# Performance work log

Hardware: AMD Instinct MI355X
Metric: run time of the kernel (lower is better)

The kernel has to match this reference:

```python
import jax, jax.numpy as jnp
import numpy as np

NE, NPROC, E, D = 50000, 25000, 200000, 128
L, T = 3, 4  # layers, edge types: 0:e->e, 1:e->p, 2:p->p, 3:p->e


def setup_inputs() -> dict:
    key = jax.random.key(0)
    ks = jax.random.split(key, 17)
    s = 1.0 / np.sqrt(D)
    return {
        'x_elem': jax.random.normal(ks[0], (NE, D), jnp.float32),
        'x_proc': jax.random.normal(ks[1], (NPROC, D), jnp.float32),
        'W_src': jax.random.normal(ks[2], (L, T, D, D), jnp.float32) * s,
        'W_dst': jax.random.normal(ks[3], (L, T, D, D), jnp.float32) * s,
        'att_src': jax.random.normal(ks[4], (L, T, D), jnp.float32) * s,
        'att_dst': jax.random.normal(ks[5], (L, T, D), jnp.float32) * s,
        'bias': jax.random.normal(ks[6], (L, T, D), jnp.float32) * 0.01,
        'lin_W': jax.random.normal(ks[7], (D, 2), jnp.float32) * s,
        'lin_b': jnp.zeros((2,), jnp.float32),
        'ee_src': jax.random.randint(ks[8], (E,), 0, NE),
        'ee_dst': jax.random.randint(ks[9], (E,), 0, NE),
        'ep_src': jax.random.randint(ks[10], (E,), 0, NE),
        'ep_dst': jax.random.randint(ks[11], (E,), 0, NPROC),
        'pp_src': jax.random.randint(ks[12], (E,), 0, NPROC),
        'pp_dst': jax.random.randint(ks[13], (E,), 0, NPROC),
        'pe_src': jax.random.randint(ks[14], (E,), 0, NPROC),
        'pe_dst': jax.random.randint(ks[15], (E,), 0, NE),
    }


def _gat(x_s, x_d, src, dst, n_dst, Ws, Wd, a_s, a_d, b):
    # one GATConv (heads=1, negative_slope=0 -> relu, no self loops)
    hs = x_s @ Ws                       # [Ns, D]
    hd = x_d @ Wd                       # [Nd, D]
    es = hs @ a_s                       # [Ns]
    ed = hd @ a_d                       # [Nd]
    logit = jax.nn.relu(es[src] + ed[dst])              # [E]
    m = jax.ops.segment_max(logit, dst, num_segments=n_dst)
    m = jnp.where(jnp.isfinite(m), m, 0.0)              # empty segments
    w = jnp.exp(logit - m[dst])
    denom = jax.ops.segment_sum(w, dst, num_segments=n_dst)
    alpha = w / jnp.maximum(denom[dst], 1e-16)          # edge softmax per dst
    out = jax.ops.segment_sum(alpha[:, None] * hs[src], dst, num_segments=n_dst)
    return out + b


def reference(x_elem, x_proc, W_src, W_dst, att_src, att_dst, bias, lin_W, lin_b,
              ee_src, ee_dst, ep_src, ep_dst, pp_src, pp_dst, pe_src, pe_dst):
    xe, xp = x_elem, x_proc
    for l in range(L):
        ee = _gat(xe, xe, ee_src, ee_dst, NE, W_src[l, 0], W_dst[l, 0], att_src[l, 0], att_dst[l, 0], bias[l, 0])
        ep = _gat(xe, xp, ep_src, ep_dst, NPROC, W_src[l, 1], W_dst[l, 1], att_src[l, 1], att_dst[l, 1], bias[l, 1])
        pp = _gat(xp, xp, pp_src, pp_dst, NPROC, W_src[l, 2], W_dst[l, 2], att_src[l, 2], att_dst[l, 2], bias[l, 2])
        pe = _gat(xp, xe, pe_src, pe_dst, NE, W_src[l, 3], W_dst[l, 3], att_src[l, 3], att_dst[l, 3], bias[l, 3])
        xe = ee + pe   # to_hetero aggr='sum' per destination node type
        xp = ep + pp
    x = jnp.concatenate([xe, xp], axis=0) @ lin_W + lin_b  # G_aggr
    return x.mean(axis=0)  # [2]
```

## Files before the change

### kernel.cpp

```cpp
#include <hip/hip_runtime.h>

#define NE_N 50000
#define NP_N 25000
#define E_N 200000
#define DIM 128
#define LOG2E 1.4426950408889634f
#define NREP 1024

#define NCHK 32
#define CHK_E (E_N / NCHK)
#define TBL 16384

typedef __attribute__((ext_vector_type(8))) short short8;
typedef __attribute__((ext_vector_type(4))) float f32x4;
typedef __attribute__((ext_vector_type(2))) float f32x2;

static __device__ __forceinline__ ushort f2bf(float f) {
  unsigned x = __float_as_uint(f);
  return (ushort)((x + 0x7fffu + ((x >> 16) & 1u)) >> 16);
}
static __device__ __forceinline__ float bf2f(ushort u) {
  return __uint_as_float(((unsigned)u) << 16);
}

#define HIST_BLKS (4 * NCHK)
#define HS_TOT (HIST_BLKS + 12 + 3)
__global__ __launch_bounds__(512) void hist_setup_k(
    const float* __restrict__ W_src, const float* __restrict__ W_dst,
    const float* __restrict__ att_dst, ushort* __restrict__ WbT,
    float* __restrict__ vec, const int* __restrict__ d0,
    const int* __restrict__ d1, const int* __restrict__ d2,
    const int* __restrict__ d3, unsigned char* __restrict__ h0,
    unsigned char* __restrict__ h1, unsigned char* __restrict__ h2,
    unsigned char* __restrict__ h3, ushort* __restrict__ rk0,
    ushort* __restrict__ rk1, ushort* __restrict__ rk2,
    ushort* __restrict__ rk3) {
  __shared__ int keys[TBL];
  __shared__ int cnts[TBL];
  const int blk = blockIdx.x;
  const int tid = threadIdx.x;
  if (blk < HIST_BLKS) {
    const int ty = blk >> 5, c = blk & (NCHK - 1);
    const int NN = (ty == 0 || ty == 3) ? NE_N : NP_N;
    const int* dst = ty == 0 ? d0 : ty == 1 ? d1 : ty == 2 ? d2 : d3;
    unsigned char* h = ty == 0 ? h0 : ty == 1 ? h1 : ty == 2 ? h2 : h3;
    ushort* rk = ty == 0 ? rk0 : ty == 1 ? rk1 : ty == 2 ? rk2 : rk3;
    for (int i = tid; i < TBL; i += 512) { keys[i] = -1; cnts[i] = 0; }
    __syncthreads();
    const int base = c * CHK_E;
    for (int i = tid; i < CHK_E; i += 512) {
      const int e = base + i;
      const int d = dst[e];
      unsigned hsh = ((unsigned)d * 2654435761u) >> 18;
      hsh &= (TBL - 1);
      int lr;
      while (true) {
        int prev = atomicCAS(&keys[hsh], -1, d);
        if (prev == -1 || prev == d) { lr = atomicAdd(&cnts[hsh], 1); break; }
        hsh = (hsh + 1) & (TBL - 1);
      }
      rk[e] = (ushort)lr;
    }
    __syncthreads();
    for (int i = tid; i < TBL; i += 512) {
      int k = keys[i];
      if (k >= 0) h[(size_t)c * NN + k] = (unsigned char)cnts[i];
    }
  } else if (blk < HIST_BLKS + 12) {
    const int w = blk - HIST_BLKS;
    const float* src = W_src + (size_t)w * DIM * DIM;
    ushort* dstw = WbT + (size_t)w * DIM * DIM;
    for (int i = tid; i < DIM * DIM; i += 512) {
      int k = i >> 7, n = i & 127;
      dstw[n * DIM + k] = f2bf(src[i]);
    }
  } else {
    const int b = blk - HIST_BLKS - 12;
    const int lt = b * 4 + (tid >> 7);
    const int i = tid & 127;
    const float* Wd = W_dst + (size_t)lt * DIM * DIM;
    const float* ad = att_dst + lt * DIM;
    float s = 0.f;
#pragma unroll 8
    for (int j = 0; j < DIM; j++) s += Wd[i * DIM + j] * ad[j];
    vec[lt * DIM + i] = s;
  }
}

__global__ __launch_bounds__(256) void scanA_k(
    unsigned char* __restrict__ h0, unsigned char* __restrict__ h1,
    unsigned char* __restrict__ h2, unsigned char* __restrict__ h3,
    int* __restrict__ c0, int* __restrict__ c1, int* __restrict__ c2,
    int* __restrict__ c3, int* __restrict__ part) {
  int ty = blockIdx.y;
  unsigned char* h = ty == 0 ? h0 : ty == 1 ? h1 : ty == 2 ? h2 : h3;
  int* cnt = ty == 0 ? c0 : ty == 1 ? c1 : ty == 2 ? c2 : c3;
  int n = (ty == 0 || ty == 3) ? NE_N : NP_N;
  int nblk = (n + 1023) >> 10;
  if ((int)blockIdx.x >= nblk) return;
  int base = blockIdx.x * 1024 + threadIdx.x * 4;
  int s = 0;
  if (base < n) {
    int run0 = 0, run1 = 0, run2 = 0, run3 = 0;
#pragma unroll
    for (int c = 0; c < NCHK; c++) {
      unsigned* hp = (unsigned*)(h + (size_t)c * n + base);
      unsigned v = *hp;
      *hp = (unsigned)(run0 & 255) | ((unsigned)(run1 & 255) << 8) |
            ((unsigned)(run2 & 255) << 16) | ((unsigned)(run3 & 255) << 24);
      run0 += (int)(v & 255u);
      run1 += (int)((v >> 8) & 255u);
      run2 += (int)((v >> 16) & 255u);
      run3 += (int)((v >> 24) & 255u);
    }
    cnt[base + 0] = run0; cnt[base + 1] = run1;
    cnt[base + 2] = run2; cnt[base + 3] = run3;
    s = run0 + run1 + run2 + run3;
  }
  int lane = threadIdx.x & 63, wid = threadIdx.x >> 6;
#pragma unroll
  for (int off = 32; off > 0; off >>= 1) s += __shfl_xor(s, off, 64);
  __shared__ int ws4[4];
  if (lane == 0) ws4[wid] = s;
  __syncthreads();
  if (threadIdx.x == 0)
    part[ty * 64 + blockIdx.x] = ws4[0] + ws4[1] + ws4[2] + ws4[3];
}

__global__ __launch_bounds__(256) void scanBC_k(
    const int* __restrict__ c0, const int* __restrict__ c1,
    const int* __restrict__ c2, const int* __restrict__ c3,
    int* __restrict__ r0, int* __restrict__ r1, int* __restrict__ r2,
    int* __restrict__ r3, const int* __restrict__ part) {
  int ty = blockIdx.y;
  int bx = blockIdx.x;
  const int* cnt = ty == 0 ? c0 : ty == 1 ? c1 : ty == 2 ? c2 : c3;
  int* rp = ty == 0 ? r0 : ty == 1 ? r1 : ty == 2 ? r2 : r3;
  int n = (ty == 0 || ty == 3) ? NE_N : NP_N;
  int nblk = (n + 1023) >> 10;
  if (bx >= nblk) return;

  __shared__ int s_excl;
  if (threadIdx.x < 64) {
    int pl = threadIdx.x;
    int v = (pl < nblk) ? part[ty * 64 + pl] : 0;
    int sc = v;
#pragma unroll
    for (int off = 1; off < 64; off <<= 1) {
      int t = __shfl_up(sc, off, 64);
      if (pl >= off) sc += t;
    }
    if (pl == bx) s_excl = sc - v;
  }
  if (bx == 0 && threadIdx.x == 0) rp[n] = E_N;
  __syncthreads();

  int base = bx * 1024 + threadIdx.x * 4;
  int v[4];
#pragma unroll
  for (int j = 0; j < 4; j++) v[j] = (base + j < n) ? cnt[base + j] : 0;
  int s = v[0] + v[1] + v[2] + v[3];
  int lane = threadIdx.x & 63, wid = threadIdx.x >> 6;
  int sc = s;
#pragma unroll
  for (int off = 1; off < 64; off <<= 1) {
    int t = __shfl_up(sc, off, 64);
    if (lane >= off) sc += t;
  }
  __shared__ int ws4[4];
  if (lane == 63) ws4[wid] = sc;
  __syncthreads();
  int wbase = 0;
  for (int w = 0; w < wid; w++) wbase += ws4[w];
  int p = s_excl + wbase + sc - s;
#pragma unroll
  for (int j = 0; j < 4; j++) {
    if (base + j < n) rp[base + j] = p;
    p += v[j];
  }
}

#define EBLK ((NE_N + 127) / 128)
#define PBLK ((NP_N + 127) / 128)
#define GEMM_BLK (EBLK + PBLK)
#define FILL_PER_CHK 13
#define FILL_BLKS (4 * NCHK * FILL_PER_CHK)
#define HG2_TOT (GEMM_BLK + FILL_BLKS)

template <bool FP32>
static __device__ __forceinline__ void gemm_body(
    int blk, const void* __restrict__ xev, const void* __restrict__ xpv,
    const ushort* __restrict__ WbT, const float* __restrict__ att,
    const float* __restrict__ vec, int l, unsigned char* __restrict__ hsE0,
    unsigned char* __restrict__ hsE1, unsigned char* __restrict__ hsP3,
    unsigned char* __restrict__ hsP2, float* __restrict__ esE0,
    float* __restrict__ esE1, float* __restrict__ esP3,
    float* __restrict__ esP2, float* __restrict__ edEA,
    float* __restrict__ edEB, float* __restrict__ edPA,
    float* __restrict__ edPB) {
  const void* xb;
  const ushort *W0T, *W1T;
  const float *a0, *a1, *dv0, *dv1;
  unsigned char *hs0, *hs1;
  float *es0, *es1, *edA, *edB;
  int N, rbase;
  if (blk < EBLK) {
    xb = xev; N = NE_N; rbase = blk * 128;
    W0T = WbT + (size_t)(l * 4 + 0) * DIM * DIM;
    W1T = WbT + (size_t)(l * 4 + 1) * DIM * DIM;
    a0 = att + (l * 4 + 0) * DIM; a1 = att + (l * 4 + 1) * DIM;
    dv0 = vec + (l * 4 + 0) * DIM; dv1 = vec + (l * 4 + 3) * DIM;
    hs0 = hsE0; hs1 = hsE1; es0 = esE0; es1 = esE1;
    edA = edEA; edB = edEB;
  } else {
    blk -= EBLK; xb = xpv; N = NP_N; rbase = blk * 128;
    W0T = WbT + (size_t)(l * 4 + 3) * DIM * DIM;
    W1T = WbT + (size_t)(l * 4 + 2) * DIM * DIM;
    a0 = att + (l * 4 + 3) * DIM; a1 = att + (l * 4 + 2) * DIM;
    dv0 = vec + (l * 4 + 1) * DIM; dv1 = vec + (l * 4 + 2) * DIM;
    hs0 = hsP3; hs1 = hsP2; es0 = esP3; es1 = esP2;
    edA = edPA; edB = edPB;
  }

  const int wave = threadIdx.x >> 6;
  const int lane = threadIdx.x & 63;
  const int m = lane & 15, quad = lane >> 4;
  const int row0 = rbase + wave * 16;
  int rowA = row0 + m;
  if (rowA >= N) rowA = N - 1;

  float4 xraw[8];
  short8 xvv[4];
  if (FP32) {
    const float* xf32 = (const float*)xb + (size_t)rowA * DIM + quad * 8;
#pragma unroll
    for (int k0 = 0; k0 < 4; k0++) {
      xraw[2 * k0] = *(const float4*)(xf32 + k0 * 32);
      xraw[2 * k0 + 1] = *(const float4*)(xf32 + k0 * 32 + 4);
    }
  } else {
    const ushort* xb16 = (const ushort*)xb + (size_t)rowA * DIM + quad * 8;
#pragma unroll
    for (int k0 = 0; k0 < 4; k0++)
      xvv[k0] = *(const short8*)(xb16 + k0 * 32);
  }

  __shared__ short8 wlds[4096];
  {
    const int i15 = lane & 15, i4 = lane >> 4;
#pragma unroll
    for (int r = 0; r < 8; r++) {
      const int g = r * 8 + wave;
      const int set = g >> 5, k0 = (g >> 3) & 3, f = g & 7;
      const ushort* WT = set ? W1T : W0T;
      wlds[g * 64 + lane] = *(const short8*)(
          WT + (size_t)(f * 16 + i15) * DIM + k0 * 32 + i4 * 8);
    }
  }
  __syncthreads();
  if (row0 >= N) return;

  float edp0 = 0.f, edp1 = 0.f;
#pragma unroll
  for (int k0 = 0; k0 < 4; k0++) {
    float xf[8];
    if (FP32) {
      float4 f0 = xraw[2 * k0], f1 = xraw[2 * k0 + 1];
      xf[0] = f0.x; xf[1] = f0.y; xf[2] = f0.z; xf[3] = f0.w;
      xf[4] = f1.x; xf[5] = f1.y; xf[6] = f1.z; xf[7] = f1.w;
      short8 xv;
#pragma unroll
      for (int j = 0; j < 8; j++) xv[j] = (short)f2bf(xf[j]);
      xvv[k0] = xv;
    } else {
#pragma unroll
      for (int j = 0; j < 8; j++) xf[j] = bf2f((ushort)xvv[k0][j]);
    }
    int off = k0 * 32 + quad * 8;
    float4 vA0 = *(const float4*)&dv0[off];
    float4 vA1 = *(const float4*)&dv0[off + 4];
    float4 vB0 = *(const float4*)&dv1[off];
    float4 vB1 = *(const float4*)&dv1[off + 4];
    edp0 += xf[0] * vA0.x + xf[1] * vA0.y + xf[2] * vA0.z + xf[3] * vA0.w +
            xf[4] * vA1.x + xf[5] * vA1.y + xf[6] * vA1.z + xf[7] * vA1.w;
    edp1 += xf[0] * vB0.x + xf[1] * vB0.y + xf[2] * vB0.z + xf[3] * vB0.w +
            xf[4] * vB1.x + xf[5] * vB1.y + xf[6] * vB1.z + xf[7] * vB1.w;
  }

  f32x4 acc0[8], acc1[8];
#pragma unroll
  for (int f = 0; f < 8; f++) {
    acc0[f] = (f32x4){0.f, 0.f, 0.f, 0.f};
    acc1[f] = (f32x4){0.f, 0.f, 0.f, 0.f};
  }
#pragma unroll
  for (int k0 = 0; k0 < 4; k0++) {
    const short8 xv = xvv[k0];
#pragma unroll
    for (int f = 0; f < 8; f++) {
      acc0[f] = __builtin_amdgcn_mfma_f32_16x16x32_bf16(
          wlds[(k0 * 8 + f) * 64 + lane], xv, acc0[f], 0, 0, 0);
      acc1[f] = __builtin_amdgcn_mfma_f32_16x16x32_bf16(
          wlds[2048 + (k0 * 8 + f) * 64 + lane], xv, acc1[f], 0, 0, 0);
    }
  }

  const int row = row0 + m;
  edp0 += __shfl_xor(edp0, 16, 64);
  edp0 += __shfl_xor(edp0, 32, 64);
  edp1 += __shfl_xor(edp1, 16, 64);
  edp1 += __shfl_xor(edp1, 32, 64);
  if (quad == 0 && row < N) {
    edA[row] = edp0 * LOG2E;
    edB[row] = edp1 * LOG2E;
  }

#pragma unroll
  for (int set = 0; set < 2; set++) {
    f32x4* acc = set ? acc1 : acc0;
    const float* as = set ? a1 : a0;
    float* es = set ? es1 : es0;
    unsigned char* hs = set ? hs1 : hs0;

    float esum = 0.f;
#pragma unroll
    for (int f = 0; f < 8; f++) {
      float4 av = *(const float4*)&as[f * 16 + quad * 4];
      esum += acc[f][0] * av.x + acc[f][1] * av.y + acc[f][2] * av.z +
              acc[f][3] * av.w;
    }
    esum += __shfl_xor(esum, 16, 64);
    esum += __shfl_xor(esum, 32, 64);
    if (quad == 0 && row < N) es[row] = esum * LOG2E;

    if (row < N) {
#pragma unroll
      for (int f = 0; f < 8; f++) {
        int w = __builtin_amdgcn_cvt_pk_fp8_f32(acc[f][0], acc[f][1], 0, false);
        w = __builtin_amdgcn_cvt_pk_fp8_f32(acc[f][2], acc[f][3], w, true);
        *(unsigned*)&hs[(size_t)row * DIM + f * 16 + quad * 4] = (unsigned)w;
      }
    }
  }
}

__global__ __launch_bounds__(512, 4) void gemm_k(
    const ushort* __restrict__ xe, const ushort* __restrict__ xp,
    const ushort* __restrict__ WbT, const float* __restrict__ att,
    const float* __restrict__ vec, int l, unsigned char* __restrict__ hsE0,
    unsigned char* __restrict__ hsE1, unsigned char* __restrict__ hsP3,
    unsigned char* __restrict__ hsP2, float* __restrict__ esE0,
    float* __restrict__ esE1, float* __restrict__ esP3,
    float* __restrict__ esP2, float* __restrict__ edEA,
    float* __restrict__ edEB, float* __restrict__ edPA,
    float* __restrict__ edPB) {
  gemm_body<false>(blockIdx.x, xe, xp, WbT, att, vec, l, hsE0, hsE1, hsP3,
                   hsP2, esE0, esE1, esP3, esP2, edEA, edEB, edPA, edPB);
}

__global__ __launch_bounds__(512, 4) void fill_gemm0_k(
    const float* __restrict__ xe, const float* __restrict__ xp,
    const ushort* __restrict__ WbT, const float* __restrict__ att,
    const float* __restrict__ vec, unsigned char* __restrict__ hsE0,
    unsigned char* __restrict__ hsE1, unsigned char* __restrict__ hsP3,
    unsigned char* __restrict__ hsP2, float* __restrict__ esE0,
    float* __restrict__ esE1, float* __restrict__ esP3,
    float* __restrict__ esP2, float* __restrict__ edEA,
    float* __restrict__ edEB, float* __restrict__ edPA,
    float* __restrict__ edPB, const int* __restrict__ s0,
    const int* __restrict__ s1, const int* __restrict__ s2,
    const int* __restrict__ s3, const int* __restrict__ d0,
    const int* __restrict__ d1, const int* __restrict__ d2,
    const int* __restrict__ d3, const ushort* __restrict__ rk0,
    const ushort* __restrict__ rk1, const ushort* __restrict__ rk2,
    const ushort* __restrict__ rk3, const int* __restrict__ r0,
    const int* __restrict__ r1, const int* __restrict__ r2,
    const int* __restrict__ r3, const unsigned char* __restrict__ h0,
    const unsigned char* __restrict__ h1, const unsigned char* __restrict__ h2,
    const unsigned char* __restrict__ h3, ushort* __restrict__ o0,
    ushort* __restrict__ o1, ushort* __restrict__ o2,
    ushort* __restrict__ o3) {
  const int blk = blockIdx.x;
  if (blk < GEMM_BLK) {
    gemm_body<true>(blk, xe, xp, WbT, att, vec, 0, hsE0, hsE1, hsP3, hsP2,
                    esE0, esE1, esP3, esP2, edEA, edEB, edPA, edPB);
  } else {
    const int fb = blk - GEMM_BLK;
    const int x = fb & 7, q = fb >> 3;
    const int g = ((q & 15) << 3) | x;
    const int j = q >> 4;
    const int i = j * 512 + threadIdx.x;
    if (i >= CHK_E) return;
    const int ty = g >> 5, c = g & 31;
    const int e = c * CHK_E + i;
    const int NN = (ty == 0 || ty == 3) ? NE_N : NP_N;
    const int* src = ty == 0 ? s0 : ty == 1 ? s1 : ty == 2 ? s2 : s3;
    const int* dst = ty == 0 ? d0 : ty == 1 ? d1 : ty == 2 ? d2 : d3;
    const ushort* rk = ty == 0 ? rk0 : ty == 1 ? rk1 : ty == 2 ? rk2 : rk3;
    const int* rp = ty == 0 ? r0 : ty == 1 ? r1 : ty == 2 ? r2 : r3;
    const unsigned char* ho = ty == 0 ? h0 : ty == 1 ? h1 : ty == 2 ? h2 : h3;
    ushort* out = ty == 0 ? o0 : ty == 1 ? o1 : ty == 2 ? o2 : o3;
    const int dd = dst[e];
    out[rp[dd] + (int)ho[(size_t)c * NN + dd] + (int)rk[e]] =
        (ushort)src[e];
  }
}

__global__ __launch_bounds__(256) void gat_gather_all(
    const int* __restrict__ rp0, const ushort* __restrict__ ss0,
    const int* __restrict__ rp1, const ushort* __restrict__ ss1,
    const int* __restrict__ rp2, const ushort* __restrict__ ss2,
    const int* __restrict__ rp3, const ushort* __restrict__ ss3,
    const float* __restrict__ esE0, const unsigned char* __restrict__ hsE0,
    const float* __restrict__ esE1, const unsigned char* __restrict__ hsE1,
    const float* __restrict__ esP3, const unsigned char* __restrict__ hsP3,
    const float* __restrict__ esP2, const unsigned char* __restrict__ hsP2,
    const float* __restrict__ edEA, const float* __restrict__ edEB,
    const float* __restrict__ edPA, const float* __restrict__ edPB,
    const float* __restrict__ bias, int l, ushort* __restrict__ outxe,
    ushort* __restrict__ outxp, int to_csum, float* __restrict__ csum_rep) {
  const int wid = (blockIdx.x * 256 + threadIdx.x) >> 6;
  const int lane = threadIdx.x & 63;
  const int slot = lane >> 3, sub = lane & 7;
  const int half = slot >> 2;
  const int hslot = slot & 3;
  const bool active = wid < NE_N + NP_N;

  float v0 = 0.f, v1 = 0.f;
  const float *b0 = bias, *b1 = bias;
  ushort* outb = outxe;
  int node = 0;

  if (active) {
    const int *rpA, *rpB;
    const ushort *ssA, *ssB;
    const float *esA, *esB;
    const unsigned char *hsA, *hsB;
    const float *edA, *edB;
    if (wid < NE_N) {
      node = wid;
      rpA = rp0; ssA = ss0; esA = esE0; hsA = hsE0;
      rpB = rp3; ssB = ss3; esB = esP3; hsB = hsP3;
      edA = edEA; edB = edEB;
      b0 = bias + (l * 4 + 0) * DIM; b1 = bias + (l * 4 + 3) * DIM;
      outb = outxe;
    } else {
      node = wid - NE_N;
      rpA = rp1; ssA = ss1; esA = esE1; hsA = hsE1;
      rpB = rp2; ssB = ss2; esB = esP2; hsB = hsP2;
      edA = edPA; edB = edPB;
      b0 = bias + (l * 4 + 1) * DIM; b1 = bias + (l * 4 + 2) * DIM;
      outb = outxp;
    }

    const int* rp = half ? rpB : rpA;
    const ushort* ss = half ? ssB : ssA;
    const float* es = half ? esB : esA;
    const unsigned char* hs = half ? hsB : hsA;
    const float edv = half ? edB[node] : edA[node];
    const int beg = rp[node], end = rp[node + 1];

    f32x2 acc2[8];
#pragma unroll
    for (int j = 0; j < 8; j++) acc2[j] = (f32x2){0.f, 0.f};
    float sw = 0.f;

    for (int e = beg + hslot; e < end; e += 4) {
      int s = ss[e];
      float w = exp2f(fmaxf(es[s] + edv, 0.f));
      sw += w;
      f32x2 w2 = {w, w};
      uint4 h = *(const uint4*)&hs[(size_t)s * DIM + sub * 16];
      acc2[0] += w2 * __builtin_amdgcn_cvt_pk_f32_fp8((int)h.x, false);
      acc2[1] += w2 * __builtin_amdgcn_cvt_pk_f32_fp8((int)h.x, true);
      acc2[2] += w2 * __builtin_amdgcn_cvt_pk_f32_fp8((int)h.y, false);
      acc2[3] += w2 * __builtin_amdgcn_cvt_pk_f32_fp8((int)h.y, true);
      acc2[4] += w2 * __builtin_amdgcn_cvt_pk_f32_fp8((int)h.z, false);
      acc2[5] += w2 * __builtin_amdgcn_cvt_pk_f32_fp8((int)h.z, true);
      acc2[6] += w2 * __builtin_amdgcn_cvt_pk_f32_fp8((int)h.w, false);
      acc2[7] += w2 * __builtin_amdgcn_cvt_pk_f32_fp8((int)h.w, true);
    }

    sw += __shfl_xor(sw, 8, 64);
    sw += __shfl_xor(sw, 16, 64);
    const float inv = 1.f / fmaxf(sw, 1e-16f);
    const f32x2 inv2 = {inv, inv};

    f32x2 res2[8];
#pragma unroll
    for (int j = 0; j < 8; j++) res2[j] = acc2[j] * inv2;

#pragma unroll
    for (int j = 0; j < 8; j++) {
      f32x2 t;
      t.x = __shfl_xor(res2[j].x, 8, 64);
      t.y = __shfl_xor(res2[j].y, 8, 64);
      res2[j] += t;
      t.x = __shfl_xor(res2[j].x, 16, 64);
      t.y = __shfl_xor(res2[j].y, 16, 64);
      res2[j] += t;
      t.x = __shfl_xor(res2[j].x, 32, 64);
      t.y = __shfl_xor(res2[j].y, 32, 64);
      res2[j] += t;
    }
    v0 = res2[slot].x;
    v1 = res2[slot].y;
  }

  const int d = sub * 16 + slot * 2;
  if (to_csum) {
    __shared__ float lsum[4][DIM];
    const int wv = threadIdx.x >> 6;
    lsum[wv][d] = v0;
    lsum[wv][d + 1] = v1;
    __syncthreads();
    if (threadIdx.x < DIM) {
      float s = lsum[0][threadIdx.x] + lsum[1][threadIdx.x] +
                lsum[2][threadIdx.x] + lsum[3][threadIdx.x];
      float* rep = csum_rep + (size_t)(blockIdx.x & (NREP - 1)) * DIM;
      unsafeAtomicAdd(&rep[threadIdx.x], s);
    }
  } else if (active) {
    float2 bb0 = *(const float2*)&b0[d];
    float2 bb1 = *(const float2*)&b1[d];
    ushort2 o;
    o.x = f2bf(v0 + bb0.x + bb1.x);
    o.y = f2bf(v1 + bb0.y + bb1.y);
    *(ushort2*)&outb[(size_t)node * DIM + d] = o;
  }
}

__global__ __launch_bounds__(512) void final_proj(
    const float* __restrict__ csum_rep, const float* __restrict__ bias,
    const float* __restrict__ lin_W, const float* __restrict__ lin_b,
    float* __restrict__ out) {
  __shared__ float parts[4][DIM];
  __shared__ float col[DIM];
  const int k = threadIdx.x & 127;
  const int pt = threadIdx.x >> 7;
  float s = 0.f;
#pragma unroll 8
  for (int r = pt * (NREP / 4); r < (pt + 1) * (NREP / 4); r++)
    s += csum_rep[(size_t)r * DIM + k];
  parts[pt][k] = s;
  __syncthreads();
  if (threadIdx.x < DIM) {
    const float* bE0 = bias + (2 * 4 + 0) * DIM;
    const float* bE1 = bias + (2 * 4 + 3) * DIM;
    const float* bP0 = bias + (2 * 4 + 1) * DIM;
    const float* bP1 = bias + (2 * 4 + 2) * DIM;
    col[k] = parts[0][k] + parts[1][k] + parts[2][k] + parts[3][k] +
             (float)NE_N * (bE0[k] + bE1[k]) +
             (float)NP_N * (bP0[k] + bP1[k]);
  }
  __syncthreads();
  if (threadIdx.x < 2) {
    float acc = 0.f;
#pragma unroll 8
    for (int j = 0; j < DIM; j++) acc += col[j] * lin_W[j * 2 + threadIdx.x];
    out[threadIdx.x] = acc / (float)(NE_N + NP_N) + lin_b[threadIdx.x];
  }
}

extern "C" void kernel_launch(void* const* d_in, const int* in_sizes, int n_in,
                              void* d_out, int out_size, void* d_ws,
                              size_t ws_size, hipStream_t stream) {
  const float* x_elem  = (const float*)d_in[0];
  const float* x_proc  = (const float*)d_in[1];
  const float* W_src   = (const float*)d_in[2];
  const float* W_dst   = (const float*)d_in[3];
  const float* att_src = (const float*)d_in[4];
  const float* att_dst = (const float*)d_in[5];
  const float* bias    = (const float*)d_in[6];
  const float* lin_W   = (const float*)d_in[7];
  const float* lin_b   = (const float*)d_in[8];
  const int* esrc[4] = {(const int*)d_in[9],  (const int*)d_in[11],
                        (const int*)d_in[13], (const int*)d_in[15]};
  const int* edst[4] = {(const int*)d_in[10], (const int*)d_in[12],
                        (const int*)d_in[14], (const int*)d_in[16]};

  char* p = (char*)d_ws;
  ushort* xe_bf[2]; ushort* xp_bf[2];
  xe_bf[0] = (ushort*)p; p += (size_t)NE_N * DIM * 2;
  xe_bf[1] = (ushort*)p; p += (size_t)NE_N * DIM * 2;
  xp_bf[0] = (ushort*)p; p += (size_t)NP_N * DIM * 2;
  xp_bf[1] = (ushort*)p; p += (size_t)NP_N * DIM * 2;
  unsigned char* hsE0 = (unsigned char*)p; p += (size_t)NE_N * DIM;
  unsigned char* hsE1 = (unsigned char*)p; p += (size_t)NE_N * DIM;
  unsigned char* hsP3 = (unsigned char*)p; p += (size_t)NP_N * DIM;
  unsigned char* hsP2 = (unsigned char*)p; p += (size_t)NP_N * DIM;
  ushort* WbT = (ushort*)p; p += (size_t)12 * DIM * DIM * 2;
  float* esE0 = (float*)p; p += (size_t)NE_N * 4;
  float* esE1 = (float*)p; p += (size_t)NE_N * 4;
  float* esP3 = (float*)p; p += (size_t)NP_N * 4;
  float* esP2 = (float*)p; p += (size_t)NP_N * 4;
  float* edEA = (float*)p; p += (size_t)NE_N * 4;
  float* edEB = (float*)p; p += (size_t)NE_N * 4;
  float* edPA = (float*)p; p += (size_t)NP_N * 4;
  float* edPB = (float*)p; p += (size_t)NP_N * 4;
  float* vec = (float*)p; p += 12 * DIM * 4;
  int* parti = (int*)p; p += 4 * 64 * 4;
  float* csum_rep = (float*)p; p += (size_t)NREP * DIM * 4;
  unsigned char* hh[4];
  hh[0] = (unsigned char*)p; p += (size_t)NE_N * NCHK;
  hh[1] = (unsigned char*)p; p += (size_t)NP_N * NCHK;
  hh[2] = (unsigned char*)p; p += (size_t)NP_N * NCHK;
  hh[3] = (unsigned char*)p; p += (size_t)NE_N * NCHK;
  int* cnt[4];
  for (int t = 0; t < 4; t++) { cnt[t] = (int*)p; p += (NE_N + 4) * 4; }
  int* rp[4];
  for (int t = 0; t < 4; t++) { rp[t] = (int*)p; p += (NE_N + 4) * 4; }
  ushort* ssrc[4];
  for (int t = 0; t < 4; t++) { ssrc[t] = (ushort*)p; p += (size_t)E_N * 2; }
  ushort* rank[4];
  for (int t = 0; t < 4; t++) { rank[t] = (ushort*)p; p += (size_t)E_N * 2; }

  hipMemsetAsync(csum_rep, 0,
                 (size_t)NREP * DIM * 4 +
                     (size_t)(2 * NE_N + 2 * NP_N) * NCHK,
                 stream);

  hist_setup_k<<<HS_TOT, 512, 0, stream>>>(
      W_src, W_dst, att_dst, WbT, vec, edst[0], edst[1], edst[2], edst[3],
      hh[0], hh[1], hh[2], hh[3], rank[0], rank[1], rank[2], rank[3]);

  scanA_k<<<dim3(49, 4), 256, 0, stream>>>(hh[0], hh[1], hh[2], hh[3],
                                           cnt[0], cnt[1], cnt[2], cnt[3],
                                           parti);
  scanBC_k<<<dim3(49, 4), 256, 0, stream>>>(cnt[0], cnt[1], cnt[2], cnt[3],
                                            rp[0], rp[1], rp[2], rp[3], parti);

  fill_gemm0_k<<<HG2_TOT, 512, 0, stream>>>(
      x_elem, x_proc, WbT, att_src, vec, hsE0, hsE1, hsP3, hsP2, esE0, esE1,
      esP3, esP2, edEA, edEB, edPA, edPB, esrc[0], esrc[1], esrc[2], esrc[3],
      edst[0], edst[1], edst[2], edst[3], rank[0], rank[1], rank[2], rank[3],
      rp[0], rp[1], rp[2], rp[3], hh[0], hh[1], hh[2], hh[3],
      ssrc[0], ssrc[1], ssrc[2], ssrc[3]);

  int c = 0;
  for (int l = 0; l < 3; l++) {
    if (l > 0) {
      gemm_k<<<GEMM_BLK, 512, 0, stream>>>(
          xe_bf[c], xp_bf[c], WbT, att_src, vec, l, hsE0, hsE1, hsP3, hsP2,
          esE0, esE1, esP3, esP2, edEA, edEB, edPA, edPB);
    }
    int to_csum = (l == 2) ? 1 : 0;
    gat_gather_all<<<(NE_N + NP_N) / 4, 256, 0, stream>>>(
        rp[0], ssrc[0], rp[1], ssrc[1], rp[2], ssrc[2], rp[3], ssrc[3], esE0,
        hsE0, esE1, hsE1, esP3, hsP3, esP2, hsP2, edEA, edEB, edPA, edPB,
        bias, l, xe_bf[1 - c], xp_bf[1 - c], to_csum, csum_rep);
    c = 1 - c;
  }

  final_proj<<<1, 512, 0, stream>>>(csum_rep, bias, lin_W, lin_b,
                                    (float*)d_out);
}
```

Measured before the change: 393.5 us.

## Process two row strips per GEMM block, async LDS weight loads, LDS transpose reduction

The GEMM blocks now cover 256 rows instead of 128, so each staged weight tile is reused across two strips. The second strip's x rows are prefetched before the first strip's compute (bf16 path) or between the two strips (fp32 path). Weight staging uses global_load_lds to write straight into LDS without passing through registers. In the gather kernel, the 24-shuffle butterfly reduction over slots is replaced with a swizzled LDS transpose and sum, which adds LDS traffic and a larger shared footprint.

```diff
diff --git a/kernel.cpp b/kernel.cpp
--- a/kernel.cpp
+++ b/kernel.cpp
@@ -21,6 +21,12 @@
 }
 static __device__ __forceinline__ float bf2f(ushort u) {
   return __uint_as_float(((unsigned)u) << 16);
+}
+
+static __device__ __forceinline__ void gload_lds16(const void* g, void* l) {
+  __builtin_amdgcn_global_load_lds(
+      (const __attribute__((address_space(1))) void*)g,
+      (__attribute__((address_space(3))) void*)l, 16, 0, 0);
 }
 
 #define HIST_BLKS (4 * NCHK)
@@ -180,12 +186,120 @@
   }
 }
 
-#define EBLK ((NE_N + 127) / 128)
-#define PBLK ((NP_N + 127) / 128)
+#define EBLK ((NE_N + 255) / 256)
+#define PBLK ((NP_N + 255) / 256)
 #define GEMM_BLK (EBLK + PBLK)
 #define FILL_PER_CHK 13
 #define FILL_BLKS (4 * NCHK * FILL_PER_CHK)
 #define HG2_TOT (GEMM_BLK + FILL_BLKS)
+
+template <bool FP32>
+static __device__ __forceinline__ void x_prefetch(
+    const void* xb, int rowA, int quad, float4* xraw, short8* xvv) {
+  if (FP32) {
+    const float* xf32 = (const float*)xb + (size_t)rowA * DIM + quad * 8;
+#pragma unroll
+    for (int k0 = 0; k0 < 4; k0++) {
+      xraw[2 * k0] = *(const float4*)(xf32 + k0 * 32);
+      xraw[2 * k0 + 1] = *(const float4*)(xf32 + k0 * 32 + 4);
+    }
+  } else {
+    const ushort* xb16 = (const ushort*)xb + (size_t)rowA * DIM + quad * 8;
+#pragma unroll
+    for (int k0 = 0; k0 < 4; k0++)
+      xvv[k0] = *(const short8*)(xb16 + k0 * 32);
+  }
+}
+
+template <bool FP32>
+static __device__ __forceinline__ void strip_body(
+    int row0, int N, int m, int quad, int lane, const short8* wlds,
+    const float* dv0, const float* dv1, const float* a0, const float* a1,
+    unsigned char* hs0, unsigned char* hs1, float* es0, float* es1,
+    float* edA, float* edB, float4* xraw, short8* xvv) {
+  float edp0 = 0.f, edp1 = 0.f;
+#pragma unroll
+  for (int k0 = 0; k0 < 4; k0++) {
+    float xf[8];
+    if (FP32) {
+      float4 f0 = xraw[2 * k0], f1 = xraw[2 * k0 + 1];
+      xf[0] = f0.x; xf[1] = f0.y; xf[2] = f0.z; xf[3] = f0.w;
+      xf[4] = f1.x; xf[5] = f1.y; xf[6] = f1.z; xf[7] = f1.w;
+      short8 xv;
+#pragma unroll
+      for (int j = 0; j < 8; j++) xv[j] = (short)f2bf(xf[j]);
+      xvv[k0] = xv;
+    } else {
+#pragma unroll
+      for (int j = 0; j < 8; j++) xf[j] = bf2f((ushort)xvv[k0][j]);
+    }
+    int off = k0 * 32 + quad * 8;
+    float4 vA0 = *(const float4*)&dv0[off];
+    float4 vA1 = *(const float4*)&dv0[off + 4];
+    float4 vB0 = *(const float4*)&dv1[off];
+    float4 vB1 = *(const float4*)&dv1[off + 4];
+    edp0 += xf[0] * vA0.x + xf[1] * vA0.y + xf[2] * vA0.z + xf[3] * vA0.w +
+            xf[4] * vA1.x + xf[5] * vA1.y + xf[6] * vA1.z + xf[7] * vA1.w;
+    edp1 += xf[0] * vB0.x + xf[1] * vB0.y + xf[2] * vB0.z + xf[3] * vB0.w +
+            xf[4] * vB1.x + xf[5] * vB1.y + xf[6] * vB1.z + xf[7] * vB1.w;
+  }
+
+  f32x4 acc0[8], acc1[8];
+#pragma unroll
+  for (int f = 0; f < 8; f++) {
+    acc0[f] = (f32x4){0.f, 0.f, 0.f, 0.f};
+    acc1[f] = (f32x4){0.f, 0.f, 0.f, 0.f};
+  }
+#pragma unroll
+  for (int k0 = 0; k0 < 4; k0++) {
+    const short8 xv = xvv[k0];
+#pragma unroll
+    for (int f = 0; f < 8; f++) {
+      acc0[f] = __builtin_amdgcn_mfma_f32_16x16x32_bf16(
+          wlds[(k0 * 8 + f) * 64 + lane], xv, acc0[f], 0, 0, 0);
+      acc1[f] = __builtin_amdgcn_mfma_f32_16x16x32_bf16(
+          wlds[2048 + (k0 * 8 + f) * 64 + lane], xv, acc1[f], 0, 0, 0);
+    }
+  }
+
+  const int row = row0 + m;
+  edp0 += __shfl_xor(edp0, 16, 64);
+  edp0 += __shfl_xor(edp0, 32, 64);
+  edp1 += __shfl_xor(edp1, 16, 64);
+  edp1 += __shfl_xor(edp1, 32, 64);
+  if (quad == 0 && row < N) {
+    edA[row] = edp0 * LOG2E;
+    edB[row] = edp1 * LOG2E;
+  }
+
+#pragma unroll
+  for (int set = 0; set < 2; set++) {
+    f32x4* acc = set ? acc1 : acc0;
+    const float* as = set ? a1 : a0;
+    float* es = set ? es1 : es0;
+    unsigned char* hs = set ? hs1 : hs0;
+
+    float esum = 0.f;
+#pragma unroll
+    for (int f = 0; f < 8; f++) {
+      float4 av = *(const float4*)&as[f * 16 + quad * 4];
+      esum += acc[f][0] * av.x + acc[f][1] * av.y + acc[f][2] * av.z +
+              acc[f][3] * av.w;
+    }
+    esum += __shfl_xor(esum, 16, 64);
+    esum += __shfl_xor(esum, 32, 64);
+    if (quad == 0 && row < N) es[row] = esum * LOG2E;
+
+    if (row < N) {
+#pragma unroll
+      for (int f = 0; f < 8; f++) {
+        int w = __builtin_amdgcn_cvt_pk_fp8_f32(acc[f][0], acc[f][1], 0, false);
+        w = __builtin_amdgcn_cvt_pk_fp8_f32(acc[f][2], acc[f][3], w, true);
+        *(unsigned*)&hs[(size_t)row * DIM + f * 16 + quad * 4] = (unsigned)w;
+      }
+    }
+  }
+}
 
 template <bool FP32>
 static __device__ __forceinline__ void gemm_body(
@@ -205,7 +319,7 @@
   float *es0, *es1, *edA, *edB;
   int N, rbase;
   if (blk < EBLK) {
-    xb = xev; N = NE_N; rbase = blk * 128;
+    xb = xev; N = NE_N; rbase = blk * 256;
     W0T = WbT + (size_t)(l * 4 + 0) * DIM * DIM;
     W1T = WbT + (size_t)(l * 4 + 1) * DIM * DIM;
     a0 = att + (l * 4 + 0) * DIM; a1 = att + (l * 4 + 1) * DIM;
@@ -213,7 +327,7 @@
     hs0 = hsE0; hs1 = hsE1; es0 = esE0; es1 = esE1;
     edA = edEA; edB = edEB;
   } else {
-    blk -= EBLK; xb = xpv; N = NP_N; rbase = blk * 128;
+    blk -= EBLK; xb = xpv; N = NP_N; rbase = blk * 256;
     W0T = WbT + (size_t)(l * 4 + 3) * DIM * DIM;
     W1T = WbT + (size_t)(l * 4 + 2) * DIM * DIM;
     a0 = att + (l * 4 + 3) * DIM; a1 = att + (l * 4 + 2) * DIM;
@@ -225,25 +339,13 @@
   const int wave = threadIdx.x >> 6;
   const int lane = threadIdx.x & 63;
   const int m = lane & 15, quad = lane >> 4;
-  const int row0 = rbase + wave * 16;
-  int rowA = row0 + m;
-  if (rowA >= N) rowA = N - 1;
-
-  float4 xraw[8];
-  short8 xvv[4];
-  if (FP32) {
-    const float* xf32 = (const float*)xb + (size_t)rowA * DIM + quad * 8;
-#pragma unroll
-    for (int k0 = 0; k0 < 4; k0++) {
-      xraw[2 * k0] = *(const float4*)(xf32 + k0 * 32);
-      xraw[2 * k0 + 1] = *(const float4*)(xf32 + k0 * 32 + 4);
-    }
-  } else {
-    const ushort* xb16 = (const ushort*)xb + (size_t)rowA * DIM + quad * 8;
-#pragma unroll
-    for (int k0 = 0; k0 < 4; k0++)
-      xvv[k0] = *(const short8*)(xb16 + k0 * 32);
-  }
+  const int row0A = rbase + wave * 16;
+  const int row0B = rbase + 128 + wave * 16;
+  int rowLA = row0A + m; if (rowLA >= N) rowLA = N - 1;
+  int rowLB = row0B + m; if (rowLB >= N) rowLB = N - 1;
+
+  float4 xrawA[8]; short8 xvvA[4];
+  x_prefetch<FP32>(xb, rowLA, quad, xrawA, xvvA);
 
   __shared__ short8 wlds[4096];
   {
@@ -253,95 +355,22 @@
       const int g = r * 8 + wave;
       const int set = g >> 5, k0 = (g >> 3) & 3, f = g & 7;
       const ushort* WT = set ? W1T : W0T;
-      wlds[g * 64 + lane] = *(const short8*)(
-          WT + (size_t)(f * 16 + i15) * DIM + k0 * 32 + i4 * 8);
+      gload_lds16(WT + (size_t)(f * 16 + i15) * DIM + k0 * 32 + i4 * 8,
+                  &wlds[g * 64]);
     }
   }
   __syncthreads();
-  if (row0 >= N) return;
-
-  float edp0 = 0.f, edp1 = 0.f;
-#pragma unroll
-  for (int k0 = 0; k0 < 4; k0++) {
-    float xf[8];
-    if (FP32) {
-      float4 f0 = xraw[2 * k0], f1 = xraw[2 * k0 + 1];
-      xf[0] = f0.x; xf[1] = f0.y; xf[2] = f0.z; xf[3] = f0.w;
-      xf[4] = f1.x; xf[5] = f1.y; xf[6] = f1.z; xf[7] = f1.w;
-      short8 xv;
-#pragma unroll
-      for (int j = 0; j < 8; j++) xv[j] = (short)f2bf(xf[j]);
-      xvv[k0] = xv;
-    } else {
-#pragma unroll
-      for (int j = 0; j < 8; j++) xf[j] = bf2f((ushort)xvv[k0][j]);
-    }
-    int off = k0 * 32 + quad * 8;
-    float4 vA0 = *(const float4*)&dv0[off];
-    float4 vA1 = *(const float4*)&dv0[off + 4];
-    float4 vB0 = *(const float4*)&dv1[off];
-    float4 vB1 = *(const float4*)&dv1[off + 4];
-    edp0 += xf[0] * vA0.x + xf[1] * vA0.y + xf[2] * vA0.z + xf[3] * vA0.w +
-            xf[4] * vA1.x + xf[5] * vA1.y + xf[6] * vA1.z + xf[7] * vA1.w;
-    edp1 += xf[0] * vB0.x + xf[1] * vB0.y + xf[2] * vB0.z + xf[3] * vB0.w +
-            xf[4] * vB1.x + xf[5] * vB1.y + xf[6] * vB1.z + xf[7] * vB1.w;
-  }
-
-  f32x4 acc0[8], acc1[8];
-#pragma unroll
-  for (int f = 0; f < 8; f++) {
-    acc0[f] = (f32x4){0.f, 0.f, 0.f, 0.f};
-    acc1[f] = (f32x4){0.f, 0.f, 0.f, 0.f};
-  }
-#pragma unroll
-  for (int k0 = 0; k0 < 4; k0++) {
-    const short8 xv = xvv[k0];
-#pragma unroll
-    for (int f = 0; f < 8; f++) {
-      acc0[f] = __builtin_amdgcn_mfma_f32_16x16x32_bf16(
-          wlds[(k0 * 8 + f) * 64 + lane], xv, acc0[f], 0, 0, 0);
-      acc1[f] = __builtin_amdgcn_mfma_f32_16x16x32_bf16(
-          wlds[2048 + (k0 * 8 + f) * 64 + lane], xv, acc1[f], 0, 0, 0);
-    }
-  }
-
-  const int row = row0 + m;
-  edp0 += __shfl_xor(edp0, 16, 64);
-  edp0 += __shfl_xor(edp0, 32, 64);
-  edp1 += __shfl_xor(edp1, 16, 64);
-  edp1 += __shfl_xor(edp1, 32, 64);
-  if (quad == 0 && row < N) {
-    edA[row] = edp0 * LOG2E;
-    edB[row] = edp1 * LOG2E;
-  }
-
-#pragma unroll
-  for (int set = 0; set < 2; set++) {
-    f32x4* acc = set ? acc1 : acc0;
-    const float* as = set ? a1 : a0;
-    float* es = set ? es1 : es0;
-    unsigned char* hs = set ? hs1 : hs0;
-
-    float esum = 0.f;
-#pragma unroll
-    for (int f = 0; f < 8; f++) {
-      float4 av = *(const float4*)&as[f * 16 + quad * 4];
-      esum += acc[f][0] * av.x + acc[f][1] * av.y + acc[f][2] * av.z +
-              acc[f][3] * av.w;
-    }
-    esum += __shfl_xor(esum, 16, 64);
-    esum += __shfl_xor(esum, 32, 64);
-    if (quad == 0 && row < N) es[row] = esum * LOG2E;
-
-    if (row < N) {
-#pragma unroll
-      for (int f = 0; f < 8; f++) {
-        int w = __builtin_amdgcn_cvt_pk_fp8_f32(acc[f][0], acc[f][1], 0, false);
-        w = __builtin_amdgcn_cvt_pk_fp8_f32(acc[f][2], acc[f][3], w, true);
-        *(unsigned*)&hs[(size_t)row * DIM + f * 16 + quad * 4] = (unsigned)w;
-      }
-    }
-  }
+
+  float4 xrawB[8]; short8 xvvB[4];
+  if (!FP32) x_prefetch<FP32>(xb, rowLB, quad, xrawB, xvvB);
+
+  if (row0A < N)
+    strip_body<FP32>(row0A, N, m, quad, lane, wlds, dv0, dv1, a0, a1,
+                     hs0, hs1, es0, es1, edA, edB, xrawA, xvvA);
+  if (FP32) x_prefetch<FP32>(xb, rowLB, quad, xrawB, xvvB);
+  if (row0B < N)
+    strip_body<FP32>(row0B, N, m, quad, lane, wlds, dv0, dv1, a0, a1,
+                     hs0, hs1, es0, es1, edA, edB, xrawB, xvvB);
 }
 
 __global__ __launch_bounds__(512, 4) void gemm_k(
@@ -419,8 +448,10 @@
     const float* __restrict__ edPA, const float* __restrict__ edPB,
     const float* __restrict__ bias, int l, ushort* __restrict__ outxe,
     ushort* __restrict__ outxp, int to_csum, float* __restrict__ csum_rep) {
+  __shared__ float2 trx[4][8][64];
   const int wid = (blockIdx.x * 256 + threadIdx.x) >> 6;
   const int lane = threadIdx.x & 63;
+  const int wv = threadIdx.x >> 6;
   const int slot = lane >> 3, sub = lane & 7;
   const int half = slot >> 2;
   const int hslot = slot & 3;
@@ -484,33 +515,25 @@
     sw += __shfl_xor(sw, 8, 64);
     sw += __shfl_xor(sw, 16, 64);
     const float inv = 1.f / fmaxf(sw, 1e-16f);
-    const f32x2 inv2 = {inv, inv};
-
-    f32x2 res2[8];
-#pragma unroll
-    for (int j = 0; j < 8; j++) res2[j] = acc2[j] * inv2;
-
-#pragma unroll
-    for (int j = 0; j < 8; j++) {
-      f32x2 t;
-      t.x = __shfl_xor(res2[j].x, 8, 64);
-      t.y = __shfl_xor(res2[j].y, 8, 64);
-      res2[j] += t;
-      t.x = __shfl_xor(res2[j].x, 16, 64);
-      t.y = __shfl_xor(res2[j].y, 16, 64);
-      res2[j] += t;
-      t.x = __shfl_xor(res2[j].x, 32, 64);
-      t.y = __shfl_xor(res2[j].y, 32, 64);
-      res2[j] += t;
-    }
-    v0 = res2[slot].x;
-    v1 = res2[slot].y;
+
+#pragma unroll
+    for (int j = 0; j < 8; j++)
+      trx[wv][slot][(sub * 8 + j) ^ slot] =
+          make_float2(acc2[j].x * inv, acc2[j].y * inv);
+    float2 vv = trx[wv][0][(sub * 8 + slot) ^ 0];
+#pragma unroll
+    for (int s2 = 1; s2 < 8; s2++) {
+      float2 t = trx[wv][s2][(sub * 8 + slot) ^ s2];
+      vv.x += t.x;
+      vv.y += t.y;
+    }
+    v0 = vv.x;
+    v1 = vv.y;
   }
 
   const int d = sub * 16 + slot * 2;
   if (to_csum) {
     __shared__ float lsum[4][DIM];
-    const int wv = threadIdx.x >> 6;
     lsum[wv][d] = v0;
     lsum[wv][d + 1] = v1;
     __syncthreads();
```

After: 382.7 us. 1.03x faster.
